# Kernel tuning notes

Measured on AMD Instinct MI355X. Metric: run time of the kernel, lower is better.

The kernel has to match this reference:

```python
import jax, jax.numpy as jnp
import numpy as np

B, P, L = 8, 196, 80
DIM1, DIM2, ATT = 2048, 300, 1024


def setup_inputs() -> dict:
    key = jax.random.key(0)
    ks = jax.random.split(key, 8)
    s1 = 1.0 / np.sqrt(DIM1)
    s2 = 1.0 / np.sqrt(DIM2)
    sa = 1.0 / np.sqrt(ATT)
    return {
        "x1": jax.random.normal(ks[0], (B, P, DIM1), dtype=jnp.float32),
        "x2": jax.random.normal(ks[1], (B, L, DIM2), dtype=jnp.float32),
        "W1": jax.random.uniform(ks[2], (DIM1, ATT), jnp.float32, -s1, s1),
        "W2": jax.random.uniform(ks[3], (DIM2, ATT), jnp.float32, -s2, s2),
        "Wh": jax.random.uniform(ks[4], (ATT, ATT), jnp.float32, -sa, sa),
        "bh": jax.random.uniform(ks[5], (ATT,), jnp.float32, -sa, sa),
        "Wt": jax.random.uniform(ks[6], (ATT,), jnp.float32, -sa, sa),
        "bt": jax.random.uniform(ks[7], (), jnp.float32, -sa, sa),
    }


def reference(x1, x2, W1, W2, Wh, bh, Wt, bt):
    # linear1 / linear2 (no bias)
    a1 = jnp.einsum('bpd,da->bpa', x1, W1)            # (B, P, ATT)
    a2 = jnp.einsum('bld,da->bla', x2, W2)            # (B, L, ATT)
    u = jnp.tanh(a1[:, None, :, :] * a2[:, :, None, :])  # (B, L, P, ATT)
    # target_linear(hidden_linear(u)) folded: u @ (Wh @ Wt) + (bh @ Wt + bt)
    w = Wh @ Wt                                        # (ATT,)
    score = jnp.einsum('blpa,a->blp', u, w) + (bh @ Wt + bt)  # (B, L, P)
    alpha = jax.nn.softmax(score, axis=-1)             # (B, L, P)
    label_repr = jnp.einsum('blp,bpd->bld', alpha, x1)  # (B, L, DIM1)
    return (label_repr, alpha)
```

## Files before the change

kernel.cpp:

```cpp
#include <hip/hip_runtime.h>
#include <math.h>

#define B_   8
#define P_   196
#define L_   80
#define DIM1 2048
#define DIM2 300
#define ATT  1024

typedef __attribute__((ext_vector_type(8))) short short8_t;
typedef __attribute__((ext_vector_type(4))) float f32x4_t;

__device__ inline unsigned short f2bf(float f) {
    unsigned int u = __float_as_uint(f);
    u += 0x7fff + ((u >> 16) & 1);
    return (unsigned short)(u >> 16);
}
__device__ inline float bf2f(unsigned short h) {
    return __uint_as_float(((unsigned int)h) << 16);
}

__global__ __launch_bounds__(256) void prep_w(const float* __restrict__ Wh,
                                              const float* __restrict__ bh,
                                              const float* __restrict__ Wt,
                                              const float* __restrict__ btp,
                                              float* __restrict__ w,
                                              float* __restrict__ biasp) {
    const int tid  = threadIdx.x;
    const int lane = tid & 63;
    const int row  = blockIdx.x * 4 + (tid >> 6);
    const float* src = (row < ATT) ? (Wh + (size_t)row * ATT) : bh;
    if (row <= ATT) {
        float acc = 0.0f;
#pragma unroll
        for (int it = 0; it < ATT / 256; ++it) {
            const int i = it * 256 + lane * 4;
            const float4 a = *reinterpret_cast<const float4*>(src + i);
            const float4 b = *reinterpret_cast<const float4*>(Wt + i);
            acc = fmaf(a.x, b.x, acc);
            acc = fmaf(a.y, b.y, acc);
            acc = fmaf(a.z, b.z, acc);
            acc = fmaf(a.w, b.w, acc);
        }
#pragma unroll
        for (int o = 32; o >= 1; o >>= 1) acc += __shfl_xor(acc, o);
        if (lane == 0) {
            if (row < ATT) {
                w[row] = acc;
                atomicAdd(&biasp[1], acc);
            } else {
                atomicAdd(&biasp[1], acc + btp[0]);
            }
        }
    }
}

__global__ __launch_bounds__(256) void tcast_all(const float* __restrict__ W1,
                                                 const float* __restrict__ W2,
                                                 unsigned short* __restrict__ W1T,
                                                 unsigned short* __restrict__ W2T) {
    __shared__ unsigned short tile[32][34];
    int id = blockIdx.x;
    const float* in;
    unsigned short* out;
    int Ksrc, Kpad, k0, n0;
    if (id < 2048) {
        in = W1; out = W1T; Ksrc = DIM1; Kpad = DIM1;
        k0 = (id & 63) * 32; n0 = (id >> 6) * 32;
    } else {
        id -= 2048;
        in = W2; out = W2T; Ksrc = DIM2; Kpad = 320;
        k0 = (id % 10) * 32; n0 = (id / 10) * 32;
    }
    const int tx = threadIdx.x & 31, ty = threadIdx.x >> 5;
#pragma unroll
    for (int i = 0; i < 4; ++i) {
        const int r = k0 + ty + i * 8;
        const float v = (r < Ksrc) ? in[(size_t)r * 1024 + n0 + tx] : 0.f;
        tile[ty + i * 8][tx] = f2bf(v);
    }
    __syncthreads();
#pragma unroll
    for (int i = 0; i < 4; ++i) {
        const int n = ty + i * 8;
        out[(size_t)(n0 + n) * Kpad + k0 + tx] = tile[tx][n];
    }
}

template<int KSRC, int KPAD>
__global__ __launch_bounds__(256) void gemm_bf16(const float* __restrict__ Af,
                                                 const unsigned short* __restrict__ Bt,
                                                 unsigned short* __restrict__ C,
                                                 int M) {
    constexpr int NT = KPAD / 64;
    __shared__ __align__(16) char smem[32768];
    const int tid  = threadIdx.x;
    const int lane = tid & 63;
    const int wave = tid >> 6;
    const int wm = (wave >> 1) * 32;
    const int wn = (wave & 1) * 32;
    const int m0 = blockIdx.y * 64;
    const int n0 = blockIdx.x * 64;

    const int row = tid >> 2;
    const int kc  = (tid & 3) * 16;
    const int swz = (row & 7) << 4;
    const int sb  = row * 128 + kc * 2;
    const int gm  = m0 + row;

    float4   ra[4];
    short8_t rb[2];

    auto LOAD = [&](int t) {
        const int k0 = t * 64;
        if (gm < M && k0 + 64 <= KSRC) {
            const float* ap = Af + (size_t)gm * KSRC + k0 + kc;
            ra[0] = *reinterpret_cast<const float4*>(ap);
            ra[1] = *reinterpret_cast<const float4*>(ap + 4);
            ra[2] = *reinterpret_cast<const float4*>(ap + 8);
            ra[3] = *reinterpret_cast<const float4*>(ap + 12);
        } else {
            float* rf = reinterpret_cast<float*>(ra);
#pragma unroll
            for (int j = 0; j < 16; ++j) {
                const int k = k0 + kc + j;
                rf[j] = (gm < M && k < KSRC) ? Af[(size_t)gm * KSRC + k] : 0.f;
            }
        }
        const unsigned short* bp = Bt + (size_t)(n0 + row) * KPAD + k0 + kc;
        rb[0] = *reinterpret_cast<const short8_t*>(bp);
        rb[1] = *reinterpret_cast<const short8_t*>(bp + 8);
    };

    auto WRITE = [&](int buf) {
        char* smA = smem + buf * 16384;
        char* smB = smA + 8192;
        const float* rf = reinterpret_cast<const float*>(ra);
        short8_t h0, h1;
#pragma unroll
        for (int j = 0; j < 8; ++j) h0[j] = (short)f2bf(rf[j]);
#pragma unroll
        for (int j = 0; j < 8; ++j) h1[j] = (short)f2bf(rf[8 + j]);
        *reinterpret_cast<short8_t*>(smA + ((sb)      ^ swz)) = h0;
        *reinterpret_cast<short8_t*>(smA + ((sb + 16) ^ swz)) = h1;
        *reinterpret_cast<short8_t*>(smB + ((sb)      ^ swz)) = rb[0];
        *reinterpret_cast<short8_t*>(smB + ((sb + 16) ^ swz)) = rb[1];
    };

    f32x4_t acc[2][2] = {};
    const int fr_col = (lane >> 4) << 4;
    const int fl     = lane & 15;

    LOAD(0);
#pragma unroll 2
    for (int t = 0; t < NT; ++t) {
        const int buf = t & 1;
        WRITE(buf);
        __syncthreads();
        if (t + 1 < NT) LOAD(t + 1);
        const char* smA = smem + buf * 16384;
        const char* smB = smA + 8192;
#pragma unroll
        for (int kk = 0; kk < 2; ++kk) {
            short8_t af[2], bf[2];
#pragma unroll
            for (int i = 0; i < 2; ++i) {
                const int r = wm + i * 16 + fl;
                af[i] = *reinterpret_cast<const short8_t*>(
                    smA + ((r * 128 + kk * 64 + fr_col) ^ ((r & 7) << 4)));
            }
#pragma unroll
            for (int j = 0; j < 2; ++j) {
                const int r = wn + j * 16 + fl;
                bf[j] = *reinterpret_cast<const short8_t*>(
                    smB + ((r * 128 + kk * 64 + fr_col) ^ ((r & 7) << 4)));
            }
#pragma unroll
            for (int i = 0; i < 2; ++i)
#pragma unroll
                for (int j = 0; j < 2; ++j)
                    acc[i][j] = __builtin_amdgcn_mfma_f32_16x16x32_bf16(af[i], bf[j], acc[i][j], 0, 0, 0);
        }
        __syncthreads();
    }

#pragma unroll
    for (int i = 0; i < 2; ++i) {
        const int gmb = m0 + wm + i * 16 + ((lane >> 4) << 2);
#pragma unroll
        for (int j = 0; j < 2; ++j) {
            const int gn = n0 + wn + j * 16 + fl;
#pragma unroll
            for (int q = 0; q < 4; ++q) {
                const int gmq = gmb + q;
                if (gmq < M) C[(size_t)gmq * 1024 + gn] = f2bf(acc[i][j][q]);
            }
        }
    }
}

__global__ __launch_bounds__(256) void score_part(const unsigned short* __restrict__ a1b,
                                                  const unsigned short* __restrict__ a2b,
                                                  const float* __restrict__ w,
                                                  const float* __restrict__ biasp,
                                                  float* __restrict__ scb) {
    __shared__ float2 aw[ATT];
    const int tid  = threadIdx.x;
    const int lane = tid & 63;
    const int wave = tid >> 6;
    const int b    = blockIdx.x & 7;
    const int rest = blockIdx.x >> 3;
    const int l    = rest >> 2;
    const int qtr  = rest & 3;
    const float bias2 = biasp[1];

    const unsigned short* a2p = a2b + (size_t)(b * L_ + l) * ATT;
    for (int i = tid; i < ATT; i += 256) {
        const float a2v = bf2f(a2p[i]);
        const int li = i & 511;
        const int phi = (i & ~511) | (((li & 7) << 6) + (li >> 3));
        aw[phi] = make_float2(a2v * 2.885390082f, w[i]);
    }
    __syncthreads();

    const int base = qtr * 49;
    float* scp = scb + (size_t)(b * L_ + l) * P_;

    for (int g = wave; g < 13; g += 4) {
        const int p0 = base + g * 4;
        int r[4];
#pragma unroll
        for (int q = 0; q < 4; ++q) r[q] = min(p0 + q, P_ - 1);
        float acc[4] = {0.f, 0.f, 0.f, 0.f};
#pragma unroll
        for (int it = 0; it < 2; ++it) {
            uint4 v[4];
#pragma unroll
            for (int q = 0; q < 4; ++q)
                v[q] = *reinterpret_cast<const uint4*>(
                    a1b + (size_t)(b * P_ + r[q]) * ATT + it * 512 + lane * 8);
#pragma unroll
            for (int h = 0; h < 4; ++h) {
                const float2 c0 = aw[it * 512 + (2 * h + 0) * 64 + lane];
                const float2 c1 = aw[it * 512 + (2 * h + 1) * 64 + lane];
#pragma unroll
                for (int q = 0; q < 4; ++q) {
                    const unsigned int u = (&v[q].x)[h];
                    const float flo = __uint_as_float(u << 16);
                    const float fhi = __uint_as_float(u & 0xffff0000u);
                    const float elo = __builtin_amdgcn_exp2f(flo * c0.x);
                    acc[q] = fmaf(c0.y, __builtin_amdgcn_rcpf(elo + 1.0f), acc[q]);
                    const float ehi = __builtin_amdgcn_exp2f(fhi * c1.x);
                    acc[q] = fmaf(c1.y, __builtin_amdgcn_rcpf(ehi + 1.0f), acc[q]);
                }
            }
        }
#pragma unroll
        for (int o = 32; o >= 1; o >>= 1) {
#pragma unroll
            for (int q = 0; q < 4; ++q) acc[q] += __shfl_xor(acc[q], o);
        }
        if (lane < 4) {
            const int p = p0 + lane;
            if (p < base + 49) scp[p] = bias2 - 2.0f * acc[lane];
        }
    }
}

__global__ __launch_bounds__(256) void label_fused(const float* __restrict__ scb,
                                                   const float* __restrict__ x1,
                                                   float* __restrict__ alpha,
                                                   float* __restrict__ out) {
    __shared__ float al[P_][4];
    const int tid  = threadIdx.x;
    const int lane = tid & 63;
    const int wave = tid >> 6;
    const int id   = blockIdx.x;
    const int b    = id & 7;
    const int rest = id >> 3;
    const int dtile = rest & 3;
    const int l0    = (rest >> 2) * 4;
    const int d0    = dtile * 512;
    const int row   = b * L_ + l0 + wave;

    const float* sp = scb + (size_t)row * P_;
    float v[4];
#pragma unroll
    for (int k = 0; k < 4; ++k) {
        const int p = lane + k * 64;
        v[k] = (p < P_) ? sp[p] : -INFINITY;
    }
    float m = fmaxf(fmaxf(v[0], v[1]), fmaxf(v[2], v[3]));
#pragma unroll
    for (int o = 32; o >= 1; o >>= 1) m = fmaxf(m, __shfl_xor(m, o));
    float e[4];
    float s = 0.f;
#pragma unroll
    for (int k = 0; k < 4; ++k) {
        const int p = lane + k * 64;
        e[k] = (p < P_) ? __expf(v[k] - m) : 0.f;
        s += e[k];
    }
#pragma unroll
    for (int o = 32; o >= 1; o >>= 1) s += __shfl_xor(s, o);
    const float inv = 1.0f / s;
    float* ap = alpha + (size_t)row * P_;
#pragma unroll
    for (int k = 0; k < 4; ++k) {
        const int p = lane + k * 64;
        if (p < P_) {
            const float a = e[k] * inv;
            al[p][wave] = a;
            if (dtile == 0) ap[p] = a;
        }
    }
    __syncthreads();

    const int d = d0 + tid * 2;
    float acc[4][2] = {};
    for (int p = 0; p < P_; ++p) {
        const float2 x = *reinterpret_cast<const float2*>(x1 + ((size_t)(b * P_ + p)) * DIM1 + d);
        const float4 a4 = *reinterpret_cast<const float4*>(&al[p][0]);
        acc[0][0] = fmaf(a4.x, x.x, acc[0][0]);
        acc[0][1] = fmaf(a4.x, x.y, acc[0][1]);
        acc[1][0] = fmaf(a4.y, x.x, acc[1][0]);
        acc[1][1] = fmaf(a4.y, x.y, acc[1][1]);
        acc[2][0] = fmaf(a4.z, x.x, acc[2][0]);
        acc[2][1] = fmaf(a4.z, x.y, acc[2][1]);
        acc[3][0] = fmaf(a4.w, x.x, acc[3][0]);
        acc[3][1] = fmaf(a4.w, x.y, acc[3][1]);
    }
#pragma unroll
    for (int l = 0; l < 4; ++l) {
        float* op = out + ((size_t)(b * L_ + l0 + l)) * DIM1 + d;
        *reinterpret_cast<float2*>(op) = make_float2(acc[l][0], acc[l][1]);
    }
}

extern "C" void kernel_launch(void* const* d_in, const int* in_sizes, int n_in,
                              void* d_out, int out_size, void* d_ws, size_t ws_size,
                              hipStream_t stream) {
    const float* x1 = (const float*)d_in[0];
    const float* x2 = (const float*)d_in[1];
    const float* W1 = (const float*)d_in[2];
    const float* W2 = (const float*)d_in[3];
    const float* Wh = (const float*)d_in[4];
    const float* bh = (const float*)d_in[5];
    const float* Wt = (const float*)d_in[6];
    const float* bt = (const float*)d_in[7];

    float* out       = (float*)d_out;
    float* label_out = out;
    float* alpha_out = out + (size_t)B_ * L_ * DIM1;

    unsigned short* usw = (unsigned short*)d_ws;
    unsigned short* W1T = usw;
    unsigned short* a2b = usw;
    unsigned short* W2T = usw + 2097152;
    unsigned short* a1b = usw + 2424832;
    float* wv    = (float*)(usw + 4030464);
    float* biasv = wv + ATT;
    float* scb   = wv + 1028;

    hipMemsetAsync(biasv, 0, 2 * sizeof(float), stream);

    prep_w<<<ATT / 4 + 1, 256, 0, stream>>>(Wh, bh, Wt, bt, wv, biasv);

    tcast_all<<<2048 + 320, 256, 0, stream>>>(W1, W2, W1T, W2T);

    gemm_bf16<DIM1, DIM1><<<dim3(16, 25), 256, 0, stream>>>(x1, W1T, a1b, B_ * P_);
    gemm_bf16<DIM2, 320><<<dim3(16, 10), 256, 0, stream>>>(x2, W2T, a2b, B_ * L_);

    score_part<<<B_ * L_ * 4, 256, 0, stream>>>(a1b, a2b, wv, biasv, scb);

    label_fused<<<B_ * L_ * 4 / 4, 256, 0, stream>>>(scb, x1, alpha_out, label_out);
}
```

Measured before the change: 197.6 us.

## Pre-cast activations to bf16 and deepen GEMM K-tile with double register sets

The pre-pass kernel now also converts x1 and x2 to bf16 (x2 padded to 512), so the GEMMs load bf16 A operands directly instead of fp32-with-conversion. The GEMM K tile grows from 64 to 128 with two register load sets and 64KB shared memory double buffering. This halves A-operand bytes read in the GEMM and removes in-loop conversion, at the cost of an extra pass over x1 and more shared memory per block, which lowers occupancy. Padding W2/x2 to 512 adds wasted MFMA work on the small GEMM.

```diff
diff --git a/kernel.cpp b/kernel.cpp
--- a/kernel.cpp
+++ b/kernel.cpp
@@ -57,43 +57,69 @@
 
 __global__ __launch_bounds__(256) void tcast_all(const float* __restrict__ W1,
                                                  const float* __restrict__ W2,
+                                                 const float* __restrict__ x1,
+                                                 const float* __restrict__ x2,
                                                  unsigned short* __restrict__ W1T,
-                                                 unsigned short* __restrict__ W2T) {
-    __shared__ unsigned short tile[32][34];
+                                                 unsigned short* __restrict__ W2T,
+                                                 unsigned short* __restrict__ x1b,
+                                                 unsigned short* __restrict__ x2b) {
+    const int tid = threadIdx.x;
     int id = blockIdx.x;
-    const float* in;
-    unsigned short* out;
-    int Ksrc, Kpad, k0, n0;
-    if (id < 2048) {
-        in = W1; out = W1T; Ksrc = DIM1; Kpad = DIM1;
-        k0 = (id & 63) * 32; n0 = (id >> 6) * 32;
+    if (id < 2560) {
+        __shared__ unsigned short tile[32][34];
+        const float* in;
+        unsigned short* out;
+        int Ksrc, Kpad, k0, n0;
+        if (id < 2048) {
+            in = W1; out = W1T; Ksrc = DIM1; Kpad = DIM1;
+            k0 = (id & 63) * 32; n0 = (id >> 6) * 32;
+        } else {
+            id -= 2048;
+            in = W2; out = W2T; Ksrc = DIM2; Kpad = 512;
+            k0 = (id & 15) * 32; n0 = (id >> 4) * 32;
+        }
+        const int tx = tid & 31, ty = tid >> 5;
+#pragma unroll
+        for (int i = 0; i < 4; ++i) {
+            const int r = k0 + ty + i * 8;
+            const float v = (r < Ksrc) ? in[(size_t)r * 1024 + n0 + tx] : 0.f;
+            tile[ty + i * 8][tx] = f2bf(v);
+        }
+        __syncthreads();
+#pragma unroll
+        for (int i = 0; i < 4; ++i) {
+            const int n = ty + i * 8;
+            out[(size_t)(n0 + n) * Kpad + k0 + tx] = tile[tx][n];
+        }
+    } else if (id < 4128) {
+        const int row = id - 2560;
+        const float* ip = x1 + (size_t)row * DIM1 + tid * 8;
+        const float4 u0 = *reinterpret_cast<const float4*>(ip);
+        const float4 u1 = *reinterpret_cast<const float4*>(ip + 4);
+        short8_t h;
+        h[0] = (short)f2bf(u0.x); h[1] = (short)f2bf(u0.y);
+        h[2] = (short)f2bf(u0.z); h[3] = (short)f2bf(u0.w);
+        h[4] = (short)f2bf(u1.x); h[5] = (short)f2bf(u1.y);
+        h[6] = (short)f2bf(u1.z); h[7] = (short)f2bf(u1.w);
+        *reinterpret_cast<short8_t*>(x1b + (size_t)row * DIM1 + tid * 8) = h;
     } else {
-        id -= 2048;
-        in = W2; out = W2T; Ksrc = DIM2; Kpad = 320;
-        k0 = (id % 10) * 32; n0 = (id / 10) * 32;
-    }
-    const int tx = threadIdx.x & 31, ty = threadIdx.x >> 5;
-#pragma unroll
-    for (int i = 0; i < 4; ++i) {
-        const int r = k0 + ty + i * 8;
-        const float v = (r < Ksrc) ? in[(size_t)r * 1024 + n0 + tx] : 0.f;
-        tile[ty + i * 8][tx] = f2bf(v);
-    }
-    __syncthreads();
-#pragma unroll
-    for (int i = 0; i < 4; ++i) {
-        const int n = ty + i * 8;
-        out[(size_t)(n0 + n) * Kpad + k0 + tx] = tile[tx][n];
-    }
-}
-
-template<int KSRC, int KPAD>
-__global__ __launch_bounds__(256) void gemm_bf16(const float* __restrict__ Af,
+        const int row = id - 4128;
+        const int k = tid * 2;
+        float2 v = make_float2(0.f, 0.f);
+        if (k < DIM2) v = *reinterpret_cast<const float2*>(x2 + (size_t)row * DIM2 + k);
+        unsigned short* op = x2b + (size_t)row * 512 + k;
+        op[0] = f2bf(v.x);
+        op[1] = f2bf(v.y);
+    }
+}
+
+template<int KPAD>
+__global__ __launch_bounds__(256) void gemm_bf16(const unsigned short* __restrict__ A,
                                                  const unsigned short* __restrict__ Bt,
                                                  unsigned short* __restrict__ C,
                                                  int M) {
-    constexpr int NT = KPAD / 64;
-    __shared__ __align__(16) char smem[32768];
+    constexpr int NT = KPAD / 128;
+    __shared__ __align__(16) char smem[65536];
     const int tid  = threadIdx.x;
     const int lane = tid & 63;
     const int wave = tid >> 6;
@@ -103,86 +129,89 @@
     const int n0 = blockIdx.x * 64;
 
     const int row = tid >> 2;
-    const int kc  = (tid & 3) * 16;
+    const int kc  = (tid & 3) * 32;
     const int swz = (row & 7) << 4;
-    const int sb  = row * 128 + kc * 2;
+    const int sb  = row * 256 + kc * 2;
     const int gm  = m0 + row;
-
-    float4   ra[4];
-    short8_t rb[2];
-
-    auto LOAD = [&](int t) {
-        const int k0 = t * 64;
-        if (gm < M && k0 + 64 <= KSRC) {
-            const float* ap = Af + (size_t)gm * KSRC + k0 + kc;
-            ra[0] = *reinterpret_cast<const float4*>(ap);
-            ra[1] = *reinterpret_cast<const float4*>(ap + 4);
-            ra[2] = *reinterpret_cast<const float4*>(ap + 8);
-            ra[3] = *reinterpret_cast<const float4*>(ap + 12);
-        } else {
-            float* rf = reinterpret_cast<float*>(ra);
-#pragma unroll
-            for (int j = 0; j < 16; ++j) {
-                const int k = k0 + kc + j;
-                rf[j] = (gm < M && k < KSRC) ? Af[(size_t)gm * KSRC + k] : 0.f;
-            }
-        }
-        const unsigned short* bp = Bt + (size_t)(n0 + row) * KPAD + k0 + kc;
-        rb[0] = *reinterpret_cast<const short8_t*>(bp);
-        rb[1] = *reinterpret_cast<const short8_t*>(bp + 8);
-    };
-
-    auto WRITE = [&](int buf) {
-        char* smA = smem + buf * 16384;
-        char* smB = smA + 8192;
-        const float* rf = reinterpret_cast<const float*>(ra);
-        short8_t h0, h1;
-#pragma unroll
-        for (int j = 0; j < 8; ++j) h0[j] = (short)f2bf(rf[j]);
-#pragma unroll
-        for (int j = 0; j < 8; ++j) h1[j] = (short)f2bf(rf[8 + j]);
-        *reinterpret_cast<short8_t*>(smA + ((sb)      ^ swz)) = h0;
-        *reinterpret_cast<short8_t*>(smA + ((sb + 16) ^ swz)) = h1;
-        *reinterpret_cast<short8_t*>(smB + ((sb)      ^ swz)) = rb[0];
-        *reinterpret_cast<short8_t*>(smB + ((sb + 16) ^ swz)) = rb[1];
-    };
+    const bool mv = (gm < M);
+
+    const unsigned short* ap = A  + (size_t)(mv ? gm : 0) * KPAD + kc;
+    const unsigned short* bp = Bt + (size_t)(n0 + row) * KPAD + kc;
+
+    short8_t raA[4], rbA[4];
+    short8_t raB[4], rbB[4];
+
+#define LOADSET(ra, rb, t)                                                   \
+    {                                                                        \
+        const int k0 = (t) * 128;                                            \
+        _Pragma("unroll")                                                    \
+        for (int j = 0; j < 4; ++j) {                                        \
+            ra[j] = mv ? *reinterpret_cast<const short8_t*>(ap + k0 + j * 8) \
+                       : short8_t{0,0,0,0,0,0,0,0};                          \
+            rb[j] = *reinterpret_cast<const short8_t*>(bp + k0 + j * 8);     \
+        }                                                                    \
+    }
+
+#define WRITESET(ra, rb, buf)                                                \
+    {                                                                        \
+        char* smA = smem + (buf) * 32768;                                    \
+        char* smB = smA + 16384;                                             \
+        _Pragma("unroll")                                                    \
+        for (int j = 0; j < 4; ++j) {                                        \
+            *reinterpret_cast<short8_t*>(smA + ((sb + 16 * j) ^ swz)) = ra[j]; \
+            *reinterpret_cast<short8_t*>(smB + ((sb + 16 * j) ^ swz)) = rb[j]; \
+        }                                                                    \
+    }
 
     f32x4_t acc[2][2] = {};
-    const int fr_col = (lane >> 4) << 4;
-    const int fl     = lane & 15;
-
-    LOAD(0);
-#pragma unroll 2
-    for (int t = 0; t < NT; ++t) {
-        const int buf = t & 1;
-        WRITE(buf);
+    const int hi16 = (lane >> 4) << 4;
+    const int fl   = lane & 15;
+
+#define COMPUTE(buf)                                                         \
+    {                                                                        \
+        const char* smA = smem + (buf) * 32768;                              \
+        const char* smB = smA + 16384;                                       \
+        _Pragma("unroll")                                                    \
+        for (int kk = 0; kk < 4; ++kk) {                                     \
+            short8_t af[2], bf[2];                                           \
+            _Pragma("unroll")                                                \
+            for (int i = 0; i < 2; ++i) {                                    \
+                const int r = wm + i * 16 + fl;                              \
+                af[i] = *reinterpret_cast<const short8_t*>(                  \
+                    smA + ((r * 256 + kk * 64 + hi16) ^ ((r & 7) << 4)));    \
+            }                                                                \
+            _Pragma("unroll")                                                \
+            for (int j = 0; j < 2; ++j) {                                    \
+                const int r = wn + j * 16 + fl;                              \
+                bf[j] = *reinterpret_cast<const short8_t*>(                  \
+                    smB + ((r * 256 + kk * 64 + hi16) ^ ((r & 7) << 4)));    \
+            }                                                                \
+            _Pragma("unroll")                                                \
+            for (int i = 0; i < 2; ++i)                                      \
+                _Pragma("unroll")                                            \
+                for (int j = 0; j < 2; ++j)                                  \
+                    acc[i][j] = __builtin_amdgcn_mfma_f32_16x16x32_bf16(     \
+                        af[i], bf[j], acc[i][j], 0, 0, 0);                   \
+        }                                                                    \
+    }
+
+    LOADSET(raA, rbA, 0);
+    LOADSET(raB, rbB, 1);
+    for (int tp = 0; tp < NT; tp += 2) {
+        WRITESET(raA, rbA, 0);
         __syncthreads();
-        if (t + 1 < NT) LOAD(t + 1);
-        const char* smA = smem + buf * 16384;
-        const char* smB = smA + 8192;
-#pragma unroll
-        for (int kk = 0; kk < 2; ++kk) {
-            short8_t af[2], bf[2];
-#pragma unroll
-            for (int i = 0; i < 2; ++i) {
-                const int r = wm + i * 16 + fl;
-                af[i] = *reinterpret_cast<const short8_t*>(
-                    smA + ((r * 128 + kk * 64 + fr_col) ^ ((r & 7) << 4)));
-            }
-#pragma unroll
-            for (int j = 0; j < 2; ++j) {
-                const int r = wn + j * 16 + fl;
-                bf[j] = *reinterpret_cast<const short8_t*>(
-                    smB + ((r * 128 + kk * 64 + fr_col) ^ ((r & 7) << 4)));
-            }
-#pragma unroll
-            for (int i = 0; i < 2; ++i)
-#pragma unroll
-                for (int j = 0; j < 2; ++j)
-                    acc[i][j] = __builtin_amdgcn_mfma_f32_16x16x32_bf16(af[i], bf[j], acc[i][j], 0, 0, 0);
-        }
+        if (tp + 2 < NT) LOADSET(raA, rbA, tp + 2);
+        COMPUTE(0);
         __syncthreads();
-    }
+        WRITESET(raB, rbB, 1);
+        __syncthreads();
+        if (tp + 3 < NT) LOADSET(raB, rbB, tp + 3);
+        COMPUTE(1);
+        __syncthreads();
+    }
+#undef LOADSET
+#undef WRITESET
+#undef COMPUTE
 
 #pragma unroll
     for (int i = 0; i < 2; ++i) {
@@ -355,21 +384,23 @@
 
     unsigned short* usw = (unsigned short*)d_ws;
     unsigned short* W1T = usw;
-    unsigned short* a2b = usw;
     unsigned short* W2T = usw + 2097152;
-    unsigned short* a1b = usw + 2424832;
-    float* wv    = (float*)(usw + 4030464);
-    float* biasv = wv + ATT;
+    unsigned short* x1b = usw + 2621440;
+    unsigned short* a1b = usw + 5832704;
+    unsigned short* x2b = usw + 7438336;
+    unsigned short* a2b = usw + 7766016;
+    float* wv    = (float*)(usw + 8421376);
+    float* biasv = wv + 1024;
     float* scb   = wv + 1028;
 
     hipMemsetAsync(biasv, 0, 2 * sizeof(float), stream);
 
     prep_w<<<ATT / 4 + 1, 256, 0, stream>>>(Wh, bh, Wt, bt, wv, biasv);
 
-    tcast_all<<<2048 + 320, 256, 0, stream>>>(W1, W2, W1T, W2T);
-
-    gemm_bf16<DIM1, DIM1><<<dim3(16, 25), 256, 0, stream>>>(x1, W1T, a1b, B_ * P_);
-    gemm_bf16<DIM2, 320><<<dim3(16, 10), 256, 0, stream>>>(x2, W2T, a2b, B_ * L_);
+    tcast_all<<<4768, 256, 0, stream>>>(W1, W2, x1, x2, W1T, W2T, x1b, x2b);
+
+    gemm_bf16<DIM1><<<dim3(16, 25), 256, 0, stream>>>(x1b, W1T, a1b, B_ * P_);
+    gemm_bf16<512><<<dim3(16, 10), 256, 0, stream>>>(x2b, W2T, a2b, B_ * L_);
 
     score_part<<<B_ * L_ * 4, 256, 0, stream>>>(a1b, a2b, wv, biasv, scb);
 
```

New measurement: 195.0 us. No clear change (-1.3%).
